# Optimization experiments

Hardware: AMD Instinct MI355X
Metric: run time of the kernel (lower is better)

The kernel has to match this reference:

```python
import jax, jax.numpy as jnp
import numpy as np

EPS = 1e-06

def _l2_norm(t):
    # normalize over channel dim (-2): einsum('bcn,bn->bcn', t, 1/||t||_{2,dim=-2})
    inv = 1.0 / jnp.linalg.norm(t, ord=2, axis=-2)  # (B, L)
    return t * inv[:, None, :]


def setup_inputs() -> dict:
    key = jax.random.key(0)
    ks = jax.random.split(key, 8)
    B, C, D = 16, 2048, 1024  # D == d_model == Length
    s = 1.0 / np.sqrt(D)
    return {
        "x": jax.random.normal(ks[0], (B, C, D), dtype=jnp.float32),
        "Wq": jax.random.normal(ks[1], (D, D), dtype=jnp.float32) * s,
        "bq": jnp.zeros((D,), dtype=jnp.float32),
        "Wk": jax.random.normal(ks[2], (D, D), dtype=jnp.float32) * s,
        "bk": jnp.zeros((D,), dtype=jnp.float32),
        "Wv": jax.random.normal(ks[3], (D, D), dtype=jnp.float32) * s,
        "bv": jnp.zeros((D,), dtype=jnp.float32),
        "gamma": jax.random.normal(ks[4], (1,), dtype=jnp.float32) * 0.1,
    }


def reference(x, Wq, bq, Wk, bk, Wv, bv, gamma):
    B, C, L = x.shape
    # Linear layers act on last dim (torch Linear: x @ W.T + b)
    Q = x @ Wq.T + bq            # (B, C, L)
    K = x @ Wk.T + bk            # (B, C, L)
    V = x @ Wv.T + bv            # (B, C, L)
    Q = jnp.transpose(_l2_norm(Q), (0, 2, 1))  # (B, L, C)
    K = _l2_norm(K)                            # (B, C, L)
    # tailor_sum: (B, L)
    tailor_sum = 1.0 / (L + jnp.einsum('bnc,bc->bn', Q, jnp.sum(K, axis=-1) + EPS))
    # value_sum: (B, C) broadcast over L
    value_sum = jnp.sum(V, axis=-1)[:, :, None]            # (B, C, 1)
    matrix = jnp.einsum('bmn,bcn->bmc', K, V)              # (B, C, C)
    matrix_sum = value_sum + jnp.einsum('bnm,bmc->bcn', Q, matrix)  # (B, C, L)
    weight_value = matrix_sum * tailor_sum[:, None, :]     # (B, C, L)
    return x + gamma * weight_value
```

## Files before the change

### kernel.cpp

```cpp
#include <hip/hip_runtime.h>
#include <cstdint>

#define DEV static __device__ __forceinline__

typedef __attribute__((ext_vector_type(4))) float f32x4;
typedef __attribute__((ext_vector_type(4))) float fl4;
typedef __attribute__((ext_vector_type(4))) unsigned short us4;
typedef __attribute__((ext_vector_type(8))) unsigned short us8;
typedef __attribute__((ext_vector_type(2))) long l2v;

DEV float b2f(unsigned short u) {
  union { unsigned int i; float f; } c; c.i = ((unsigned int)u) << 16; return c.f;
}
DEV unsigned short f2b(float f) {
  union { float f; unsigned int i; } c; c.f = f;
  unsigned int u = c.i;
  u += 0x7fffu + ((u >> 16) & 1u);
  return (unsigned short)(u >> 16);
}
DEV unsigned int f4_to_fp8x4(float a, float b, float c, float d) {
  int r = __builtin_amdgcn_cvt_pk_fp8_f32(a, b, 0, false);
  r = __builtin_amdgcn_cvt_pk_fp8_f32(c, d, r, true);
  return (unsigned int)r;
}
DEV unsigned char f2f8(float v) {
  return (unsigned char)__builtin_amdgcn_cvt_pk_fp8_f32(v, v, 0, false);
}

DEV void gload16(const void* g, void* l) {
  __builtin_amdgcn_global_load_lds(
      (const __attribute__((address_space(1))) unsigned int*)g,
      (__attribute__((address_space(3))) unsigned int*)l, 16, 0, 0);
}

DEV float red16(float v) {
  v += __shfl_xor(v, 1); v += __shfl_xor(v, 2);
  v += __shfl_xor(v, 4); v += __shfl_xor(v, 8);
  return v;
}
DEV float red4lk(float v) {
  v += __shfl_xor(v, 16); v += __shfl_xor(v, 32);
  return v;
}

__global__ __launch_bounds__(256) void k_xcast(const float* __restrict__ src,
                                               unsigned short* __restrict__ dh,
                                               unsigned char* __restrict__ d8, long n) {
  long i = ((long)blockIdx.x * 256 + threadIdx.x) * 4;
  if (i >= n) return;
  fl4 v = *(const fl4*)(src + i);
  us4 o;
  o[0] = f2b(v[0]); o[1] = f2b(v[1]); o[2] = f2b(v[2]); o[3] = f2b(v[3]);
  *(us4*)(dh + i) = o;
  *(unsigned int*)(d8 + i) = f4_to_fp8x4(v[0], v[1], v[2], v[3]);
}

__global__ __launch_bounds__(256) void k_wcast8(const float* __restrict__ wq,
                                                const float* __restrict__ wk,
                                                const float* __restrict__ wv,
                                                unsigned char* __restrict__ dst) {
  const long i = ((long)blockIdx.x * 256 + threadIdx.x) * 4;
  const int seg = (int)(i >> 20);
  const float* s = seg == 0 ? wq : (seg == 1 ? wk : wv);
  fl4 v = *(const fl4*)(s + (i & 1048575));
  *(unsigned int*)(dst + i) = f4_to_fp8x4(v[0], v[1], v[2], v[3]);
}

__global__ __launch_bounds__(256) void k_bias_cat(const float* __restrict__ bq,
                                                  const float* __restrict__ bk,
                                                  const float* __restrict__ bv,
                                                  float* __restrict__ o) {
  const int t = blockIdx.x * 256 + threadIdx.x;
  o[t] = t < 1024 ? bq[t] : (t < 2048 ? bk[t - 1024] : bv[t - 2048]);
}

#define MFMA_FP8(A, B, C) __builtin_amdgcn_mfma_f32_16x16x32_fp8_fp8((A), (B), (C), 0, 0, 0)
#define SBAR   __builtin_amdgcn_s_barrier()

__global__ __launch_bounds__(1024, 4)
void k_g16qkv8(const unsigned char* __restrict__ A,
               const unsigned char* __restrict__ Bt,
               unsigned char* __restrict__ QT8, unsigned char* __restrict__ KT8,
               unsigned char* __restrict__ Vout8,
               int Kb,
               const float* __restrict__ bias,
               float* __restrict__ r1, float* __restrict__ r2,
               float* __restrict__ r3, float* __restrict__ r4) {
  __shared__ __align__(16) unsigned char LDSU[131072];

  const int tid = threadIdx.x;
  const int wv = tid >> 6, lane = tid & 63;
  const int wr = wv >> 2, wcn = wv & 3;
  const int l15 = lane & 15, lk = lane >> 4;

  const int nx = gridDim.x;
  const int nwg = nx * gridDim.y;
  const int lin = blockIdx.y * nx + blockIdx.x;
  const int cpx = nwg >> 3;
  const int wg = (lin & 7) * cpx + (lin >> 3);
  const int bn = wg % nx;
  const int bm = wg / nx;

  const unsigned char* Ab = A + (long)bm * 256 * Kb;
  const unsigned char* Bb = Bt + (long)bn * 256 * Kb;

  const int scsw = (tid & 3) ^ ((tid >> 3) & 3);
  const long gOff = (long)(tid >> 2) * Kb + (long)scsw * 16;
  const int ldsb = wv * 1024;

  const int rdsw = (lk ^ ((l15 >> 1) & 3)) * 16;
  const int abase = (wr * 64 + l15) * 64;
  const int bbase = (wcn * 64 + l15) * 64;

  f32x4 acc[4][4];
#pragma unroll
  for (int i = 0; i < 4; ++i)
#pragma unroll
    for (int j = 0; j < 4; ++j) acc[i][j] = (f32x4){0.f, 0.f, 0.f, 0.f};

#define STAGEQ(T, BUF)                                                        \
  {                                                                           \
    const long kb = (long)(T) * 64;                                           \
    gload16(Ab + kb + gOff, LDSU + (BUF) * 16384 + ldsb);                     \
    gload16(Bb + kb + gOff, LDSU + 65536 + (BUF) * 16384 + ldsb);             \
  }

  STAGEQ(0, 0)
  STAGEQ(1, 1)

  const int NT = Kb >> 6;
  for (int t = 0; t < NT; ++t) {
    if (t < NT - 1) { asm volatile("s_waitcnt vmcnt(2)" ::: "memory"); }
    else            { asm volatile("s_waitcnt vmcnt(0)" ::: "memory"); }
    if ((t & 1) == 0) SBAR;
    if (t + 2 < NT) STAGEQ(t + 2, (t + 2) & 3)

    const unsigned char* Asc = LDSU + (t & 3) * 16384;
    const unsigned char* Bsc = LDSU + 65536 + (t & 3) * 16384;
    l2v Bf[4], Af[4];
#pragma unroll
    for (int j = 0; j < 4; ++j)
      Bf[j] = *(const l2v*)&Bsc[bbase + j * 1024 + rdsw];
#pragma unroll
    for (int i = 0; i < 4; ++i)
      Af[i] = *(const l2v*)&Asc[abase + i * 1024 + rdsw];

    __builtin_amdgcn_s_setprio(1);
#pragma unroll
    for (int i = 0; i < 4; ++i)
#pragma unroll
      for (int j = 0; j < 4; ++j) {
        acc[i][j] = MFMA_FP8(Af[i][0], Bf[j][0], acc[i][j]);
        acc[i][j] = MFMA_FP8(Af[i][1], Bf[j][1], acc[i][j]);
      }
    __builtin_amdgcn_s_setprio(0);
  }
#undef STAGEQ
  SBAR;

  const int row0 = bm * 256 + wr * 64;
  const int col0 = bn * 256 + wcn * 64;

  const int seg = bn >> 2;
  const int b = bm >> 3;
  float bvj[4];
#pragma unroll
  for (int j = 0; j < 4; ++j) bvj[j] = bias[col0 + j * 16 + l15];
  const int colL0 = col0 & 1023;
  unsigned char* sc8 = LDSU;

  if (seg < 2) {
#pragma unroll
    for (int i = 0; i < 4; ++i)
#pragma unroll
      for (int j = 0; j < 4; ++j) {
        const int p = wcn * 64 + j * 16 + l15;
        const int m = wr * 64 + i * 16 + lk * 4;
        const unsigned int pk4 = f4_to_fp8x4(acc[i][j][0] + bvj[j], acc[i][j][1] + bvj[j],
                                             acc[i][j][2] + bvj[j], acc[i][j][3] + bvj[j]);
        *(unsigned int*)&sc8[p * 256 + (((m >> 4) ^ (p & 15)) << 4) + (m & 15)] = pk4;
      }
#pragma unroll
    for (int j = 0; j < 4; ++j) {
      const int colL = colL0 + j * 16 + l15;
      float ss = 0.f, sm = 0.f;
#pragma unroll
      for (int i = 0; i < 4; ++i)
#pragma unroll
        for (int r = 0; r < 4; ++r) {
          const float v = acc[i][j][r] + bvj[j];
          ss += v * v; sm += v;
        }
      ss = red4lk(ss);
      if (seg == 0) sm = red4lk(sm);
      if (lk == 0) {
        atomicAdd(&(seg == 0 ? r1 : r3)[(long)b * 1024 + colL], ss);
        if (seg == 0) atomicAdd(&r2[(long)b * 1024 + colL], sm);
      }
    }
    SBAR;
    unsigned char* tp = (seg == 0 ? QT8 : KT8) + (long)b * 2097152;
    const int P0 = (bn & 3) * 256;
    const int M0 = (bm & 7) * 256;
#pragma unroll
    for (int it = 0; it < 4; ++it) {
      const int p = it * 64 + (tid >> 4);
      const int c = tid & 15;
      us8 v = *(const us8*)&sc8[p * 256 + ((c ^ (p & 15)) << 4)];
      *(us8*)&tp[(long)(P0 + p) * 2048 + M0 + c * 16] = v;
    }
  } else {
#pragma unroll
    for (int i = 0; i < 4; ++i)
#pragma unroll
      for (int r = 0; r < 4; ++r) {
        const int rl = wr * 64 + i * 16 + lk * 4 + r;
        float sm = 0.f;
#pragma unroll
        for (int j = 0; j < 4; ++j) {
          const float v = acc[i][j][r] + bvj[j];
          sm += v;
          const int col = wcn * 64 + j * 16 + l15;
          sc8[rl * 256 + (((col >> 4) ^ (rl & 15)) << 4) + (col & 15)] = f2f8(v);
        }
        sm = red16(sm);
        if (l15 == 0) atomicAdd(&r4[row0 + i * 16 + lk * 4 + r], sm);
      }
    SBAR;
    const int C0 = (bn & 3) * 256;
#pragma unroll
    for (int it = 0; it < 4; ++it) {
      const int rl = it * 64 + (tid >> 4);
      const int c = tid & 15;
      us8 v = *(const us8*)&sc8[rl * 256 + ((c ^ (rl & 15)) << 4)];
      *(us8*)&Vout8[(long)(bm * 256 + rl) * 1024 + C0 + c * 16] = v;
    }
  }
}

__global__ __launch_bounds__(1024, 4)
void k_g16s8(const unsigned char* __restrict__ A,
             const unsigned char* __restrict__ Bt,
             unsigned char* __restrict__ Sout,
             int Kb,
             const float* __restrict__ pq, const float* __restrict__ pk,
             float* __restrict__ Srow) {
  __shared__ __align__(16) unsigned char LDSU[131072];

  const int tid = threadIdx.x;
  const int wv = tid >> 6, lane = tid & 63;
  const int wr = wv >> 2, wcn = wv & 3;
  const int l15 = lane & 15, lk = lane >> 4;

  const int nx = gridDim.x;
  const int nwg = nx * gridDim.y;
  const int lin = blockIdx.y * nx + blockIdx.x;
  const int cpx = nwg >> 3;
  const int wg = (lin & 7) * cpx + (lin >> 3);
  const int bn = wg % nx;
  const int bm = wg / nx;
  const int bz = blockIdx.z;

  const unsigned char* Ab = A + (long)bz * 2097152 + (long)bm * 256 * Kb;
  const unsigned char* Bb = Bt + (long)bz * 2097152 + (long)bn * 256 * Kb;

  const int scsw = (tid & 3) ^ ((tid >> 3) & 3);
  const long gOff = (long)(tid >> 2) * Kb + (long)scsw * 16;
  const int ldsb = wv * 1024;

  const int rdsw = (lk ^ ((l15 >> 1) & 3)) * 16;
  const int abase = (wr * 64 + l15) * 64;
  const int bbase = (wcn * 64 + l15) * 64;

  f32x4 acc[4][4];
#pragma unroll
  for (int i = 0; i < 4; ++i)
#pragma unroll
    for (int j = 0; j < 4; ++j) acc[i][j] = (f32x4){0.f, 0.f, 0.f, 0.f};

#define STAGES(T, BUF)                                                        \
  {                                                                           \
    const long kb = (long)(T) * 64;                                           \
    gload16(Ab + kb + gOff, LDSU + (BUF) * 16384 + ldsb);                     \
    gload16(Bb + kb + gOff, LDSU + 65536 + (BUF) * 16384 + ldsb);             \
  }

  STAGES(0, 0)
  STAGES(1, 1)

  const int NT = Kb >> 6;
  for (int t = 0; t < NT; ++t) {
    if (t < NT - 1) { asm volatile("s_waitcnt vmcnt(2)" ::: "memory"); }
    else            { asm volatile("s_waitcnt vmcnt(0)" ::: "memory"); }
    if ((t & 1) == 0) SBAR;
    if (t + 2 < NT) STAGES(t + 2, (t + 2) & 3)

    const unsigned char* Asc = LDSU + (t & 3) * 16384;
    const unsigned char* Bsc = LDSU + 65536 + (t & 3) * 16384;
    l2v Bf[4], Af[4];
#pragma unroll
    for (int j = 0; j < 4; ++j)
      Bf[j] = *(const l2v*)&Bsc[bbase + j * 1024 + rdsw];
#pragma unroll
    for (int i = 0; i < 4; ++i)
      Af[i] = *(const l2v*)&Asc[abase + i * 1024 + rdsw];

    __builtin_amdgcn_s_setprio(1);
#pragma unroll
    for (int i = 0; i < 4; ++i)
#pragma unroll
      for (int j = 0; j < 4; ++j) {
        acc[i][j] = MFMA_FP8(Af[i][0], Bf[j][0], acc[i][j]);
        acc[i][j] = MFMA_FP8(Af[i][1], Bf[j][1], acc[i][j]);
      }
    __builtin_amdgcn_s_setprio(0);
  }
#undef STAGES
  SBAR;

  const int row0 = bm * 256 + wr * 64;
  const int col0 = bn * 256 + wcn * 64;
  unsigned char* sc8 = LDSU;

  float ivk[4];
#pragma unroll
  for (int j = 0; j < 4; ++j) ivk[j] = rsqrtf(pk[bz * 1024 + col0 + j * 16 + l15]);
#pragma unroll
  for (int i = 0; i < 4; ++i)
#pragma unroll
    for (int r = 0; r < 4; ++r) {
      const int rl = wr * 64 + i * 16 + lk * 4 + r;
      const float ivq = rsqrtf(pq[bz * 1024 + row0 + i * 16 + lk * 4 + r]);
      float sm = 0.f;
#pragma unroll
      for (int j = 0; j < 4; ++j) {
        const float v = acc[i][j][r] * ivq * ivk[j];
        sm += v;
        const int col = wcn * 64 + j * 16 + l15;
        sc8[rl * 256 + (((col >> 4) ^ (rl & 15)) << 4) + (col & 15)] = f2f8(v);
      }
      sm = red16(sm);
      if (l15 == 0) atomicAdd(&Srow[(long)bz * 1024 + row0 + i * 16 + lk * 4 + r], sm);
    }
  SBAR;
  unsigned char* Cb = Sout + (long)bz * 1048576;
#pragma unroll
  for (int it = 0; it < 4; ++it) {
    const int rl = it * 64 + (tid >> 4);
    const int c = tid & 15;
    us8 v = *(const us8*)&sc8[rl * 256 + ((c ^ (rl & 15)) << 4)];
    *(us8*)&Cb[(long)(bm * 256 + rl) * 1024 + bn * 256 + c * 16] = v;
  }
}

__global__ __launch_bounds__(1024, 4)
void k_g16fin(const unsigned char* __restrict__ A,
              const unsigned char* __restrict__ Bt,
              float* __restrict__ Out,
              int Kb,
              const unsigned short* __restrict__ xh,
              const float* __restrict__ Vsum,
              const float* __restrict__ Srow,
              const float* __restrict__ pq,
              const float* __restrict__ qsum,
              const float* __restrict__ gptr) {
  __shared__ __align__(16) unsigned char LDSU[131072];

  const int tid = threadIdx.x;
  const int wv = tid >> 6, lane = tid & 63;
  const int wr = wv >> 2, wcn = wv & 3;
  const int l15 = lane & 15, lk = lane >> 4;

  const int nx = gridDim.x;
  const int nwg = nx * gridDim.y;
  const int lin = blockIdx.y * nx + blockIdx.x;
  const int cpx = nwg >> 3;
  const int wg = (lin & 7) * cpx + (lin >> 3);
  const int bn = wg % nx;
  const int bm = wg / nx;
  const int bz = blockIdx.z;

  const unsigned char* Ab = A + (long)bz * 2097152 + (long)bm * 256 * Kb;
  const unsigned char* Bb = Bt + (long)bz * 1048576 + (long)bn * 256 * Kb;

  const int scsw = (tid & 3) ^ ((tid >> 3) & 3);
  const long gOff = (long)(tid >> 2) * Kb + (long)scsw * 16;
  const int ldsb = wv * 1024;

  const int rdsw = (lk ^ ((l15 >> 1) & 3)) * 16;
  const int abase = (wr * 64 + l15) * 64;
  const int bbase = (wcn * 64 + l15) * 64;

  f32x4 acc[4][4];
#pragma unroll
  for (int i = 0; i < 4; ++i)
#pragma unroll
    for (int j = 0; j < 4; ++j) acc[i][j] = (f32x4){0.f, 0.f, 0.f, 0.f};

#define STAGEF(T, BUF)                                                        \
  {                                                                           \
    const long kb = (long)(T) * 64;                                           \
    gload16(Ab + kb + gOff, LDSU + (BUF) * 16384 + ldsb);                     \
    gload16(Bb + kb + gOff, LDSU + 65536 + (BUF) * 16384 + ldsb);             \
  }

  STAGEF(0, 0)
  STAGEF(1, 1)

  const int NT = Kb >> 6;
  for (int t = 0; t < NT; ++t) {
    if (t < NT - 1) { asm volatile("s_waitcnt vmcnt(2)" ::: "memory"); }
    else            { asm volatile("s_waitcnt vmcnt(0)" ::: "memory"); }
    if ((t & 1) == 0) SBAR;
    if (t + 2 < NT) STAGEF(t + 2, (t + 2) & 3)

    const unsigned char* Asc = LDSU + (t & 3) * 16384;
    const unsigned char* Bsc = LDSU + 65536 + (t & 3) * 16384;
    l2v Bf[4], Af[4];
#pragma unroll
    for (int j = 0; j < 4; ++j)
      Bf[j] = *(const l2v*)&Bsc[bbase + j * 1024 + rdsw];
#pragma unroll
    for (int i = 0; i < 4; ++i)
      Af[i] = *(const l2v*)&Asc[abase + i * 1024 + rdsw];

    __builtin_amdgcn_s_setprio(1);
#pragma unroll
    for (int i = 0; i < 4; ++i)
#pragma unroll
      for (int j = 0; j < 4; ++j) {
        acc[i][j] = MFMA_FP8(Af[i][0], Bf[j][0], acc[i][j]);
        acc[i][j] = MFMA_FP8(Af[i][1], Bf[j][1], acc[i][j]);
      }
    __builtin_amdgcn_s_setprio(0);
  }
#undef STAGEF
  SBAR;

  float* scf = (float*)LDSU;
  float* Cb = Out + (long)bz * 2097152;
  const float g = gptr[0];
#pragma unroll
  for (int h = 0; h < 4; ++h) {
    if (wr == h) {
#pragma unroll
      for (int i = 0; i < 4; ++i)
#pragma unroll
        for (int j = 0; j < 4; ++j) {
          const int col = wcn * 64 + j * 16 + l15;
          const int cc = col >> 2, c3 = col & 3;
#pragma unroll
          for (int r = 0; r < 4; ++r) {
            const int rl = i * 16 + lk * 4 + r;
            scf[rl * 256 + ((cc ^ (rl & 15)) << 2) + c3] = acc[i][j][r];
          }
        }
    }
    SBAR;
#pragma unroll
    for (int it = 0; it < 4; ++it) {
      const int rl = it * 16 + wv;
      const int rg = bm * 256 + h * 64 + rl;
      const int c = lane;
      fl4 a4 = *(const fl4*)&scf[rl * 256 + ((c ^ (rl & 15)) << 2)];
      const int cg = bn * 256 + c * 4;
      us4 xv = *(const us4*)&xh[((long)bz * 2048 + rg) * 1024 + cg];
      fl4 sr = *(const fl4*)&Srow[bz * 1024 + cg];
      fl4 pq4 = *(const fl4*)&pq[bz * 1024 + cg];
      fl4 qs4 = *(const fl4*)&qsum[bz * 1024 + cg];
      const float vs = Vsum[bz * 2048 + rg];
      fl4 o;
#pragma unroll
      for (int q = 0; q < 4; ++q) {
        const float tl = 1.0f / (1024.0f + sr[q] + 1e-6f * rsqrtf(pq4[q]) * qs4[q]);
        o[q] = b2f(xv[q]) + g * ((vs + a4[q]) * tl);
      }
      *(fl4*)&Cb[(long)rg * 1024 + cg] = o;
    }
    if (h < 3) SBAR;
  }
}

extern "C" void kernel_launch(void* const* d_in, const int* in_sizes, int n_in,
                              void* d_out, int out_size, void* d_ws, size_t ws_size,
                              hipStream_t stream) {
  (void)in_sizes; (void)n_in; (void)out_size;
  const float* x     = (const float*)d_in[0];
  const float* Wq    = (const float*)d_in[1];
  const float* bq    = (const float*)d_in[2];
  const float* Wk    = (const float*)d_in[3];
  const float* bk    = (const float*)d_in[4];
  const float* Wv    = (const float*)d_in[5];
  const float* bv    = (const float*)d_in[6];
  const float* gamma = (const float*)d_in[7];

  const long NE = 16L * 2048 * 1024;

  char* w = (char*)d_ws;
  unsigned char*  QT8 = (unsigned char*)(w);
  unsigned char*  KT8 = (unsigned char*)(w + 33554432L);
  unsigned char*  V8  = (unsigned char*)(w + 67108864L);
  unsigned short* xh  = (unsigned short*)(w + 100663296L);
  unsigned char*  x8  = (unsigned char*)(w + 167772160L);
  unsigned char*  S8  = (unsigned char*)(w + 201326592L);
  size_t off = 218103808L;
  unsigned char* W8   = (unsigned char*)(w + off); off += 3145728;
  char* accbase = w + off;
  float* pq     = (float*)(w + off); off += 65536;
  float* qsum   = (float*)(w + off); off += 65536;
  float* pk     = (float*)(w + off); off += 65536;
  float* Vsum   = (float*)(w + off); off += 131072;
  float* Srow   = (float*)(w + off); off += 65536;
  const size_t accbytes = (size_t)(w + off - accbase);
  float* bqkv   = (float*)(w + off); off += 12288;
  if (ws_size < off) return;

  hipMemsetAsync(accbase, 0, accbytes, stream);

  k_xcast<<<dim3((unsigned)(NE / 1024)), 256, 0, stream>>>(x, xh, x8, NE);
  k_wcast8<<<dim3(3072), 256, 0, stream>>>(Wq, Wk, Wv, W8);
  k_bias_cat<<<dim3(12), 256, 0, stream>>>(bq, bk, bv, bqkv);

  k_g16qkv8<<<dim3(12, 128, 1), 1024, 0, stream>>>(
      x8, W8, QT8, KT8, V8, 1024, bqkv, pq, qsum, pk, Vsum);

  k_g16s8<<<dim3(4, 4, 16), 1024, 0, stream>>>(
      QT8, KT8, S8, 2048, pq, pk, Srow);

  k_g16fin<<<dim3(4, 8, 16), 1024, 0, stream>>>(
      V8, S8, (float*)d_out, 1024, xh, Vsum, Srow, pq, qsum, gamma);
}
```

Before: 344.8 us.

## Software-pipeline LDS fragment reads with double-buffered registers in all three GEMMs

Restructures the main K loop of the three FP8 MFMA GEMM kernels. The next tile's LDS fragments are read into a second register set while the current tile's MFMAs run, and the loop is unrolled by two with one barrier per pair. The goal is to hide LDS read latency behind MFMA work. It costs extra VGPRs under a 1024-thread launch bound and adds a subtle ordering dependency: a 4-deep LDS ring is reused with only one barrier every two tiles.

```diff
diff --git a/kernel.cpp b/kernel.cpp
--- a/kernel.cpp
+++ b/kernel.cpp
@@ -77,6 +77,45 @@
 #define MFMA_FP8(A, B, C) __builtin_amdgcn_mfma_f32_16x16x32_fp8_fp8((A), (B), (C), 0, 0, 0)
 #define SBAR   __builtin_amdgcn_s_barrier()
 
+
+#define RDFRAGS(T, AF, BF)                                                    \
+  {                                                                           \
+    const unsigned char* Asc_ = LDSU + ((T) & 3) * 16384;                     \
+    const unsigned char* Bsc_ = LDSU + 65536 + ((T) & 3) * 16384;             \
+    _Pragma("unroll")                                                         \
+    for (int j_ = 0; j_ < 4; ++j_)                                            \
+      BF[j_] = *(const l2v*)&Bsc_[bbase + j_ * 1024 + rdsw];                  \
+    _Pragma("unroll")                                                         \
+    for (int i_ = 0; i_ < 4; ++i_)                                            \
+      AF[i_] = *(const l2v*)&Asc_[abase + i_ * 1024 + rdsw];                  \
+  }
+
+#define MFMACLUST(AC, BC)                                                     \
+  {                                                                           \
+    __builtin_amdgcn_s_setprio(1);                                            \
+    _Pragma("unroll")                                                         \
+    for (int i_ = 0; i_ < 4; ++i_)                                            \
+      _Pragma("unroll")                                                       \
+      for (int j_ = 0; j_ < 4; ++j_) {                                        \
+        acc[i_][j_] = MFMA_FP8(AC[i_][0], BC[j_][0], acc[i_][j_]);            \
+        acc[i_][j_] = MFMA_FP8(AC[i_][1], BC[j_][1], acc[i_][j_]);            \
+      }                                                                       \
+    __builtin_amdgcn_s_setprio(0);                                            \
+  }
+
+#define QBODY(T, STG, AC, BC, AN, BN)                                         \
+  {                                                                           \
+    if ((T) + 2 < NT) {                                                       \
+      STG((T) + 2, ((T) + 2) & 3)                                             \
+      asm volatile("s_waitcnt vmcnt(2)" ::: "memory");                        \
+      RDFRAGS((T) + 1, AN, BN)                                                \
+    } else if ((T) + 1 < NT) {                                                \
+      asm volatile("s_waitcnt vmcnt(0)" ::: "memory");                        \
+      RDFRAGS((T) + 1, AN, BN)                                                \
+    }                                                                         \
+    MFMACLUST(AC, BC)                                                         \
+  }
+
 __global__ __launch_bounds__(1024, 4)
 void k_g16qkv8(const unsigned char* __restrict__ A,
                const unsigned char* __restrict__ Bt,
@@ -127,33 +166,17 @@
 
   STAGEQ(0, 0)
   STAGEQ(1, 1)
+  asm volatile("s_waitcnt vmcnt(2)" ::: "memory");
+  SBAR;
+
+  l2v Ac[4], Bc[4], An[4], Bn[4];
+  RDFRAGS(0, Ac, Bc)
 
   const int NT = Kb >> 6;
-  for (int t = 0; t < NT; ++t) {
-    if (t < NT - 1) { asm volatile("s_waitcnt vmcnt(2)" ::: "memory"); }
-    else            { asm volatile("s_waitcnt vmcnt(0)" ::: "memory"); }
-    if ((t & 1) == 0) SBAR;
-    if (t + 2 < NT) STAGEQ(t + 2, (t + 2) & 3)
-
-    const unsigned char* Asc = LDSU + (t & 3) * 16384;
-    const unsigned char* Bsc = LDSU + 65536 + (t & 3) * 16384;
-    l2v Bf[4], Af[4];
-#pragma unroll
-    for (int j = 0; j < 4; ++j)
-      Bf[j] = *(const l2v*)&Bsc[bbase + j * 1024 + rdsw];
-#pragma unroll
-    for (int i = 0; i < 4; ++i)
-      Af[i] = *(const l2v*)&Asc[abase + i * 1024 + rdsw];
-
-    __builtin_amdgcn_s_setprio(1);
-#pragma unroll
-    for (int i = 0; i < 4; ++i)
-#pragma unroll
-      for (int j = 0; j < 4; ++j) {
-        acc[i][j] = MFMA_FP8(Af[i][0], Bf[j][0], acc[i][j]);
-        acc[i][j] = MFMA_FP8(Af[i][1], Bf[j][1], acc[i][j]);
-      }
-    __builtin_amdgcn_s_setprio(0);
+  for (int t = 0; t < NT; t += 2) {
+    SBAR;
+    QBODY(t,     STAGEQ, Ac, Bc, An, Bn)
+    QBODY(t + 1, STAGEQ, An, Bn, Ac, Bc)
   }
 #undef STAGEQ
   SBAR;
@@ -287,33 +310,17 @@
 
   STAGES(0, 0)
   STAGES(1, 1)
+  asm volatile("s_waitcnt vmcnt(2)" ::: "memory");
+  SBAR;
+
+  l2v Ac[4], Bc[4], An[4], Bn[4];
+  RDFRAGS(0, Ac, Bc)
 
   const int NT = Kb >> 6;
-  for (int t = 0; t < NT; ++t) {
-    if (t < NT - 1) { asm volatile("s_waitcnt vmcnt(2)" ::: "memory"); }
-    else            { asm volatile("s_waitcnt vmcnt(0)" ::: "memory"); }
-    if ((t & 1) == 0) SBAR;
-    if (t + 2 < NT) STAGES(t + 2, (t + 2) & 3)
-
-    const unsigned char* Asc = LDSU + (t & 3) * 16384;
-    const unsigned char* Bsc = LDSU + 65536 + (t & 3) * 16384;
-    l2v Bf[4], Af[4];
-#pragma unroll
-    for (int j = 0; j < 4; ++j)
-      Bf[j] = *(const l2v*)&Bsc[bbase + j * 1024 + rdsw];
-#pragma unroll
-    for (int i = 0; i < 4; ++i)
-      Af[i] = *(const l2v*)&Asc[abase + i * 1024 + rdsw];
-
-    __builtin_amdgcn_s_setprio(1);
-#pragma unroll
-    for (int i = 0; i < 4; ++i)
-#pragma unroll
-      for (int j = 0; j < 4; ++j) {
-        acc[i][j] = MFMA_FP8(Af[i][0], Bf[j][0], acc[i][j]);
-        acc[i][j] = MFMA_FP8(Af[i][1], Bf[j][1], acc[i][j]);
-      }
-    __builtin_amdgcn_s_setprio(0);
+  for (int t = 0; t < NT; t += 2) {
+    SBAR;
+    QBODY(t,     STAGES, Ac, Bc, An, Bn)
+    QBODY(t + 1, STAGES, An, Bn, Ac, Bc)
   }
 #undef STAGES
   SBAR;
@@ -406,33 +413,17 @@
 
   STAGEF(0, 0)
   STAGEF(1, 1)
+  asm volatile("s_waitcnt vmcnt(2)" ::: "memory");
+  SBAR;
+
+  l2v Ac[4], Bc[4], An[4], Bn[4];
+  RDFRAGS(0, Ac, Bc)
 
   const int NT = Kb >> 6;
-  for (int t = 0; t < NT; ++t) {
-    if (t < NT - 1) { asm volatile("s_waitcnt vmcnt(2)" ::: "memory"); }
-    else            { asm volatile("s_waitcnt vmcnt(0)" ::: "memory"); }
-    if ((t & 1) == 0) SBAR;
-    if (t + 2 < NT) STAGEF(t + 2, (t + 2) & 3)
-
-    const unsigned char* Asc = LDSU + (t & 3) * 16384;
-    const unsigned char* Bsc = LDSU + 65536 + (t & 3) * 16384;
-    l2v Bf[4], Af[4];
-#pragma unroll
-    for (int j = 0; j < 4; ++j)
-      Bf[j] = *(const l2v*)&Bsc[bbase + j * 1024 + rdsw];
-#pragma unroll
-    for (int i = 0; i < 4; ++i)
-      Af[i] = *(const l2v*)&Asc[abase + i * 1024 + rdsw];
-
-    __builtin_amdgcn_s_setprio(1);
-#pragma unroll
-    for (int i = 0; i < 4; ++i)
-#pragma unroll
-      for (int j = 0; j < 4; ++j) {
-        acc[i][j] = MFMA_FP8(Af[i][0], Bf[j][0], acc[i][j]);
-        acc[i][j] = MFMA_FP8(Af[i][1], Bf[j][1], acc[i][j]);
-      }
-    __builtin_amdgcn_s_setprio(0);
+  for (int t = 0; t < NT; t += 2) {
+    SBAR;
+    QBODY(t,     STAGEF, Ac, Bc, An, Bn)
+    QBODY(t + 1, STAGEF, An, Bn, Ac, Bc)
   }
 #undef STAGEF
   SBAR;
```

New measurement: 878.5 us. 155% more time.
